# Kernel optimization log

Measured on AMD Instinct MI355X. Metric: run time of the kernel, lower is better.

## Reference

```python
import jax, jax.numpy as jnp
import numpy as np

N, D, M = 4096, 2048, 1000
NL = 2048
MAX_ITER = 5


def setup_inputs() -> dict:
    key = jax.random.key(0)
    k1, k2, k3 = jax.random.split(key, 3)
    fc7 = jax.random.normal(k1, (N, D), dtype=jnp.float32)
    # prior probs: softmax over random logits (row-stochastic, like CNN softmax output)
    probs = jax.nn.softmax(jax.random.normal(k2, (N, M), dtype=jnp.float32), axis=-1)
    labs = jax.random.randint(k3, (NL,), 0, M)
    L = jnp.arange(NL)
    U = jnp.arange(NL, N)
    return {"fc7": fc7, "probs": probs, "labs": labs, "L": L, "U": U}


def _get_W_correlation(fc7):
    # Pearson correlation between rows, negatives clipped to zero (set_negative='hard')
    x = fc7 - fc7.mean(axis=1, keepdims=True)
    norms = jnp.linalg.norm(x, axis=1)  # [n]
    W = (x @ x.T) / jnp.outer(norms, norms)  # [n, n]
    return jax.nn.relu(W)


def _init_probs_prior(probs, labs, L, U):
    n, m = probs.shape
    ps = jnp.zeros((n, m), dtype=probs.dtype)
    ps = ps.at[U].set(probs[U])       # unlabeled: CNN prior
    ps = ps.at[L, labs].set(1.0)      # labeled: one-hot
    return ps


def _replicator(W, ps, max_iter):
    def step(p, _):
        q = p * (W @ p)                              # [n, m]
        q = q / jnp.sum(q, axis=1, keepdims=True)
        return q, None
    ps, _ = jax.lax.scan(step, ps, None, length=max_iter)
    return ps


def reference(fc7, probs, labs, L, U):
    W = _get_W_correlation(fc7)
    ps = _init_probs_prior(probs, labs, L, U)
    ps = _replicator(W, ps, MAX_ITER)
    return ps, W
```

## Files before the change

### kernel.cpp

```cpp
#include <hip/hip_runtime.h>
#include <stdint.h>

#define NS 4096
#define DD 2048
#define MC 1000
#define MP 1024
#define NLAB 2048
#define NU 2048

typedef __attribute__((ext_vector_type(8))) short bf16x8;
typedef __attribute__((ext_vector_type(4))) float f32x4;

__device__ inline unsigned short f2bf(float f) {
  union { float f; uint32_t u; } v; v.f = f;
  uint32_t u = v.u;
  u = u + 0x7fffu + ((u >> 16) & 1u);
  return (unsigned short)(u >> 16);
}
__device__ inline float bf2f(unsigned short h) {
  union { uint32_t u; float f; } v; v.u = ((uint32_t)h) << 16;
  return v.f;
}

__device__ inline void gload_lds16(const void* g, void* l) {
  __builtin_amdgcn_global_load_lds(
      (const __attribute__((address_space(1))) void*)g,
      (__attribute__((address_space(3))) void*)l, 16, 0, 0);
}

__device__ inline float block_sum(float v, float* sm, int tid) {
  #pragma unroll
  for (int o = 32; o > 0; o >>= 1) v += __shfl_down(v, o, 64);
  __syncthreads();
  if ((tid & 63) == 0) sm[tid >> 6] = v;
  __syncthreads();
  return sm[0] + sm[1] + sm[2] + sm[3];
}

__global__ void center_norm_k(const float* __restrict__ fc7,
                              unsigned short* __restrict__ Xc,
                              float* __restrict__ invn) {
  __shared__ float sm[4];
  const int row = blockIdx.x;
  const int tid = threadIdx.x;
  const float4* src = (const float4*)(fc7 + (size_t)row * DD);
  float4 a = src[tid * 2];
  float4 b = src[tid * 2 + 1];
  float s = a.x + a.y + a.z + a.w + b.x + b.y + b.z + b.w;
  s = block_sum(s, sm, tid);
  const float mean = s * (1.f / (float)DD);
  float v0 = a.x - mean, v1 = a.y - mean, v2 = a.z - mean, v3 = a.w - mean;
  float v4 = b.x - mean, v5 = b.y - mean, v6 = b.z - mean, v7 = b.w - mean;
  float ss = v0*v0 + v1*v1 + v2*v2 + v3*v3 + v4*v4 + v5*v5 + v6*v6 + v7*v7;
  ss = block_sum(ss, sm, tid);
  if (tid == 0) invn[row] = rsqrtf(ss);
  ushort4 o0 = make_ushort4(f2bf(v0), f2bf(v1), f2bf(v2), f2bf(v3));
  ushort4 o1 = make_ushort4(f2bf(v4), f2bf(v5), f2bf(v6), f2bf(v7));
  ushort4* dst = (ushort4*)(Xc + (size_t)row * DD);
  dst[tid * 2] = o0;
  dst[tid * 2 + 1] = o1;
}

__global__ void gemm_w_sym(const unsigned short* __restrict__ A,
                           const float* __restrict__ invn,
                           float* __restrict__ outF,
                           unsigned short* __restrict__ outBF) {
  __shared__ __align__(16) unsigned short As[64 * 64];
  __shared__ __align__(16) unsigned short Bs[128 * 64];
  const int tid = threadIdx.x;
  const int wv = tid >> 6;
  const int ln = tid & 63;
  const int wr = wv >> 1, wc = wv & 1;

  int b = (blockIdx.x & 7) * 132 + (blockIdx.x >> 3);
  int r = 0;
  while (b >= 32 - (r >> 1)) { b -= 32 - (r >> 1); ++r; }
  const int c = (r >> 1) + b;
  const int rowBase = r * 64;
  const int colBase = c * 128;
  const bool mirror = (c > (r >> 1));
  const bool bfStraight = (colBase >= NLAB);
  const bool bfMirror = mirror && (rowBase >= NLAB);
  const int fr = ln & 15, kg = ln >> 4;

  f32x4 acc[2][4];
  f32x4 zz = {0.f, 0.f, 0.f, 0.f};
  #pragma unroll
  for (int i = 0; i < 2; ++i)
    #pragma unroll
    for (int j = 0; j < 4; ++j) acc[i][j] = zz;

  const int lrow = ln >> 3;
  const int lcol = ((ln & 7) ^ lrow) * 8;
  const unsigned short* Ap = A + (size_t)(rowBase + lrow) * DD + lcol;
  const unsigned short* Bp = A + (size_t)(colBase + lrow) * DD + lcol;

  for (int k0 = 0; k0 < DD; k0 += 64) {
    if (k0) __syncthreads();
    #pragma unroll
    for (int u = 0; u < 2; ++u) {
      const int rr = wv * 16 + u * 8;
      gload_lds16(Ap + (size_t)rr * DD + k0, &As[rr * 64]);
    }
    #pragma unroll
    for (int u = 0; u < 4; ++u) {
      const int rr = wv * 32 + u * 8;
      gload_lds16(Bp + (size_t)rr * DD + k0, &Bs[rr * 64]);
    }
    __syncthreads();
    #pragma unroll
    for (int kk = 0; kk < 2; ++kk) {
      bf16x8 af[2], bfr[4];
      #pragma unroll
      for (int i = 0; i < 2; ++i) {
        const int rr = wr * 32 + i * 16 + fr;
        af[i] = *(const bf16x8*)&As[rr * 64 + ((kk * 4 + kg) ^ (rr & 7)) * 8];
      }
      #pragma unroll
      for (int j = 0; j < 4; ++j) {
        const int rr = wc * 64 + j * 16 + fr;
        bfr[j] = *(const bf16x8*)&Bs[rr * 64 + ((kk * 4 + kg) ^ (rr & 7)) * 8];
      }
      #pragma unroll
      for (int i = 0; i < 2; ++i)
        #pragma unroll
        for (int j = 0; j < 4; ++j)
          acc[i][j] = __builtin_amdgcn_mfma_f32_16x16x32_bf16(af[i], bfr[j], acc[i][j], 0, 0, 0);
    }
  }

  const int cr = (ln >> 4) * 4;
  const int cc = ln & 15;
  #pragma unroll
  for (int i = 0; i < 2; ++i) {
    const int rb = rowBase + wr * 32 + i * 16 + cr;
    #pragma unroll
    for (int j = 0; j < 4; ++j) {
      const int cb = colBase + wc * 64 + j * 16 + cc;
      const float ic = invn[cb];
      float v[4];
      #pragma unroll
      for (int u = 0; u < 4; ++u) {
        float x = acc[i][j][u] * invn[rb + u] * ic;
        v[u] = x > 0.f ? x : 0.f;
        const size_t o = (size_t)(rb + u) * NS + cb;
        outF[o] = v[u];
        if (bfStraight) outBF[o] = f2bf(v[u]);
      }
      if (mirror) {
        const size_t o = (size_t)cb * NS + rb;
        *(float4*)&outF[o] = make_float4(v[0], v[1], v[2], v[3]);
        if (bfMirror)
          *(ushort4*)&outBF[o] = make_ushort4(f2bf(v[0]), f2bf(v[1]), f2bf(v[2]), f2bf(v[3]));
      }
    }
  }
}

__global__ void gemm_rep(const unsigned short* __restrict__ pT,
                         const unsigned short* __restrict__ Wbf,
                         float* __restrict__ q0, float* __restrict__ q1,
                         float* __restrict__ q2, float* __restrict__ q3,
                         int kBase) {
  __shared__ __align__(16) unsigned short As[64 * 64];
  __shared__ __align__(16) unsigned short Bs[128 * 64];
  const int tid = threadIdx.x;
  const int wv = tid >> 6;
  const int ln = tid & 63;
  const int wr = wv >> 1, wc = wv & 1;
  const int rowBase = blockIdx.y * 64;
  const int colBase = blockIdx.x * 128;
  const int kOff = kBase + blockIdx.z * 512;
  float* __restrict__ outF = (blockIdx.z == 0) ? q0 : (blockIdx.z == 1) ? q1
                           : (blockIdx.z == 2) ? q2 : q3;
  const int fr = ln & 15, kg = ln >> 4;

  f32x4 acc[2][4];
  f32x4 zz = {0.f, 0.f, 0.f, 0.f};
  #pragma unroll
  for (int i = 0; i < 2; ++i)
    #pragma unroll
    for (int j = 0; j < 4; ++j) acc[i][j] = zz;

  const int lrow = ln >> 3;
  const int lcol = ((ln & 7) ^ lrow) * 8;
  const unsigned short* Ap = pT + (size_t)(rowBase + lrow) * NS + kOff + lcol;
  const unsigned short* Bp = Wbf + (size_t)(NLAB + colBase + lrow) * NS + kOff + lcol;

  for (int k0 = 0; k0 < 512; k0 += 64) {
    if (k0) __syncthreads();
    #pragma unroll
    for (int u = 0; u < 2; ++u) {
      const int rr = wv * 16 + u * 8;
      gload_lds16(Ap + (size_t)rr * NS + k0, &As[rr * 64]);
    }
    #pragma unroll
    for (int u = 0; u < 4; ++u) {
      const int rr = wv * 32 + u * 8;
      gload_lds16(Bp + (size_t)rr * NS + k0, &Bs[rr * 64]);
    }
    __syncthreads();
    #pragma unroll
    for (int kk = 0; kk < 2; ++kk) {
      bf16x8 af[2], bfr[4];
      #pragma unroll
      for (int i = 0; i < 2; ++i) {
        const int rr = wr * 32 + i * 16 + fr;
        af[i] = *(const bf16x8*)&As[rr * 64 + ((kk * 4 + kg) ^ (rr & 7)) * 8];
      }
      #pragma unroll
      for (int j = 0; j < 4; ++j) {
        const int rr = wc * 64 + j * 16 + fr;
        bfr[j] = *(const bf16x8*)&Bs[rr * 64 + ((kk * 4 + kg) ^ (rr & 7)) * 8];
      }
      #pragma unroll
      for (int i = 0; i < 2; ++i)
        #pragma unroll
        for (int j = 0; j < 4; ++j)
          acc[i][j] = __builtin_amdgcn_mfma_f32_16x16x32_bf16(af[i], bfr[j], acc[i][j], 0, 0, 0);
    }
  }

  const int cr = (ln >> 4) * 4;
  const int cc = ln & 15;
  #pragma unroll
  for (int i = 0; i < 2; ++i) {
    const int rb = rowBase + wr * 32 + i * 16 + cr;
    #pragma unroll
    for (int j = 0; j < 4; ++j) {
      const int cb = colBase + wc * 64 + j * 16 + cc;
      #pragma unroll
      for (int u = 0; u < 4; ++u)
        outF[(size_t)(rb + u) * NU + cb] = acc[i][j][u];
    }
  }
}

__global__ void wl_gather_k(const int* __restrict__ labs,
                            const unsigned short* __restrict__ Wbf,
                            float* __restrict__ WL) {
  __shared__ unsigned long long masks[32];
  const int m = blockIdx.x;
  const int t = threadIdx.x;
  const int wv = t >> 6, ln = t & 63;
  #pragma unroll
  for (int u = 0; u < 8; ++u) {
    const int w2 = wv * 8 + u;
    unsigned long long msk = __ballot(labs[w2 * 64 + ln] == m);
    if (ln == 0) masks[w2] = msk;
  }
  __syncthreads();
  float acc[8] = {0.f, 0.f, 0.f, 0.f, 0.f, 0.f, 0.f, 0.f};
  for (int w2 = 0; w2 < 32; ++w2) {
    unsigned long long m64 = masks[w2];
    while (m64) {
      const int bit = __ffsll(m64) - 1;
      m64 &= (m64 - 1);
      const int j = w2 * 64 + bit;
      bf16x8 w = *(const bf16x8*)&Wbf[(size_t)j * NS + NLAB + t * 8];
      #pragma unroll
      for (int k = 0; k < 8; ++k) acc[k] += bf2f((unsigned short)w[k]);
    }
  }
  float* dst = WL + (size_t)m * NU + t * 8;
  *(float4*)dst = make_float4(acc[0], acc[1], acc[2], acc[3]);
  *(float4*)(dst + 4) = make_float4(acc[4], acc[5], acc[6], acc[7]);
}

__global__ void init_pT_k(const float* __restrict__ probs, const int* __restrict__ labs,
                          unsigned short* __restrict__ pT) {
  __shared__ float t[32][33];
  const int tx = threadIdx.x, ty = threadIdx.y;
  const int i0 = blockIdx.x * 32, m0 = blockIdx.y * 32;
  const int i = i0 + ty;
  const int m = m0 + tx;
  float v = 0.f;
  if (i < NLAB) v = (m == labs[i]) ? 1.f : 0.f;
  else if (m < MC) v = probs[(size_t)i * MC + m];
  t[ty][tx] = v;
  __syncthreads();
  pT[(size_t)(m0 + ty) * NS + i0 + tx] = f2bf(t[tx][ty]);
}

__global__ void onehot_k(const int* __restrict__ labs, float* __restrict__ ps) {
  const int i = blockIdx.x;
  const int m4 = threadIdx.x * 4;
  if (m4 >= MC) return;
  const int lab = labs[i];
  float4 v;
  v.x = (lab == m4)     ? 1.f : 0.f;
  v.y = (lab == m4 + 1) ? 1.f : 0.f;
  v.z = (lab == m4 + 2) ? 1.f : 0.f;
  v.w = (lab == m4 + 3) ? 1.f : 0.f;
  *(float4*)&ps[(size_t)i * MC + m4] = v;
}

__global__ void colsum_part_k(const float* __restrict__ q0, const float* __restrict__ q1,
                              const float* __restrict__ q2, const float* __restrict__ q3,
                              const float* __restrict__ WL,
                              const unsigned short* __restrict__ pT,
                              float* __restrict__ pq,
                              float* __restrict__ part) {
  const int i = blockIdx.x * 256 + threadIdx.x;
  const int c = blockIdx.y;
  float s = 0.f;
  #pragma unroll 4
  for (int mm = 0; mm < 64; ++mm) {
    const int m = c * 64 + mm;
    const size_t o = (size_t)m * NU + i;
    const float q = q0[o] + q1[o] + q2[o] + q3[o] + WL[o];
    const float f = bf2f(pT[(size_t)m * NS + NLAB + i]) * q;
    s += f;
    pq[o] = f;
  }
  part[c * NU + i] = s;
}

__global__ void colsum_fin_k(const float* __restrict__ part, float* __restrict__ rsum) {
  const int i = blockIdx.x * 256 + threadIdx.x;
  float s = 0.f;
  #pragma unroll
  for (int c = 0; c < 16; ++c) s += part[c * NU + i];
  rsum[i] = 1.0f / s;
}

__global__ void scale_k(const float* __restrict__ pq,
                        const float* __restrict__ rsum,
                        unsigned short* __restrict__ pT) {
  const int g = blockIdx.x * 256 + threadIdx.x;
  const int idx = g * 4;
  const int i = idx & (NU - 1);
  const int m = idx >> 11;
  float4 p = *(const float4*)(pq + idx);
  float4 r = *(const float4*)(rsum + i);
  ushort4 o = make_ushort4(f2bf(p.x * r.x), f2bf(p.y * r.y),
                           f2bf(p.z * r.z), f2bf(p.w * r.w));
  *(ushort4*)(pT + (size_t)m * NS + NLAB + i) = o;
}

__global__ void final_k(const float* __restrict__ pq,
                        const float* __restrict__ rsum,
                        float* __restrict__ ps) {
  __shared__ float t[32][33];
  const int tx = threadIdx.x, ty = threadIdx.y;
  const int i0 = blockIdx.x * 32, m0 = blockIdx.y * 32;
  t[ty][tx] = pq[(size_t)(m0 + ty) * NU + i0 + tx];
  __syncthreads();
  const int i = i0 + ty, m = m0 + tx;
  if (m < MC)
    ps[(size_t)(NLAB + i) * MC + m] = t[tx][ty] * rsum[i];
}

extern "C" void kernel_launch(void* const* d_in, const int* in_sizes, int n_in,
                              void* d_out, int out_size, void* d_ws, size_t ws_size,
                              hipStream_t stream) {
  const float* fc7   = (const float*)d_in[0];
  const float* probs = (const float*)d_in[1];
  const int*   labs  = (const int*)d_in[2];

  char* ws = (char*)d_ws;
  unsigned short* Xc   = (unsigned short*)(ws);
  unsigned short* Wbf  = (unsigned short*)(ws + (16ull << 20));
  unsigned short* pT   = (unsigned short*)(ws + (48ull << 20));
  float*          q0   = (float*)(ws + (56ull << 20));
  float*          q1   = (float*)(ws + (64ull << 20));
  float*          q2   = (float*)(ws + (72ull << 20));
  float*          q3   = (float*)(ws + (80ull << 20));
  float*          WL   = (float*)(ws + (88ull << 20));
  float*          pq   = (float*)(ws + (96ull << 20));
  float*          invn = (float*)(ws + (104ull << 20));
  float*          rsum = (float*)(ws + (104ull << 20) + (16ull << 10));
  float*          part = (float*)(ws + (105ull << 20));

  float* out_ps = (float*)d_out;
  float* out_W  = out_ps + (size_t)NS * MC;

  center_norm_k<<<NS, 256, 0, stream>>>(fc7, Xc, invn);

  gemm_w_sym<<<1056, 256, 0, stream>>>(Xc, invn, out_W, Wbf);

  init_pT_k<<<dim3(NS / 32, MP / 32), dim3(32, 32), 0, stream>>>(probs, labs, pT);
  onehot_k<<<NLAB, 256, 0, stream>>>(labs, out_ps);

  wl_gather_k<<<MP, 256, 0, stream>>>(labs, Wbf, WL);

  for (int it = 0; it < 5; ++it) {
    gemm_rep<<<dim3(NU / 128, MP / 64, 4), 256, 0, stream>>>(pT, Wbf, q0, q1, q2, q3, NLAB);
    colsum_part_k<<<dim3(NU / 256, 16), 256, 0, stream>>>(q0, q1, q2, q3, WL, pT, pq, part);
    colsum_fin_k<<<NU / 256, 256, 0, stream>>>(part, rsum);
    if (it < 4)
      scale_k<<<(MP * NU / 4) / 256, 256, 0, stream>>>(pq, rsum, pT);
    else
      final_k<<<dim3(NU / 32, MP / 32), dim3(32, 32), 0, stream>>>(pq, rsum, out_ps);
  }
}
```

Before: 266.2 us.

## Fuse row normalization into replicator GEMM A-tile load, drop scale kernel

Removes the per-iteration scale kernel that wrote a bf16 transposed probability buffer. The replicator GEMM now reads the unnormalized fp32 product buffer plus the reciprocal row sums, multiplies and converts to bf16 while staging the A tile into shared memory. The colsum kernel applies the pending scale itself, and ping-pong buffers carry the product and sums between iterations. This saves one launch and a full read/write pass per iteration, but the GEMM now does synchronous fp32 loads (twice the bytes) with conversion instead of direct-to-LDS bf16 loads, which can slow its inner loop.

```diff
diff --git a/kernel.cpp b/kernel.cpp
--- a/kernel.cpp
+++ b/kernel.cpp
@@ -157,11 +157,11 @@
   }
 }
 
-__global__ void gemm_rep(const unsigned short* __restrict__ pT,
+__global__ void gemm_rep(const float* __restrict__ pqP,
+                         const float* __restrict__ rsP,
                          const unsigned short* __restrict__ Wbf,
                          float* __restrict__ q0, float* __restrict__ q1,
-                         float* __restrict__ q2, float* __restrict__ q3,
-                         int kBase) {
+                         float* __restrict__ q2, float* __restrict__ q3) {
   __shared__ __align__(16) unsigned short As[64 * 64];
   __shared__ __align__(16) unsigned short Bs[128 * 64];
   const int tid = threadIdx.x;
@@ -170,7 +170,7 @@
   const int wr = wv >> 1, wc = wv & 1;
   const int rowBase = blockIdx.y * 64;
   const int colBase = blockIdx.x * 128;
-  const int kOff = kBase + blockIdx.z * 512;
+  const int kU = blockIdx.z * 512;
   float* __restrict__ outF = (blockIdx.z == 0) ? q0 : (blockIdx.z == 1) ? q1
                            : (blockIdx.z == 2) ? q2 : q3;
   const int fr = ln & 15, kg = ln >> 4;
@@ -182,17 +182,30 @@
     #pragma unroll
     for (int j = 0; j < 4; ++j) acc[i][j] = zz;
 
-  const int lrow = ln >> 3;
-  const int lcol = ((ln & 7) ^ lrow) * 8;
-  const unsigned short* Ap = pT + (size_t)(rowBase + lrow) * NS + kOff + lcol;
-  const unsigned short* Bp = Wbf + (size_t)(NLAB + colBase + lrow) * NS + kOff + lcol;
+  const int lr = ln >> 3;
+  const int sg = ln & 7;
+  const int sl = sg ^ lr;
+  const unsigned short* Bp = Wbf + (size_t)(NLAB + colBase + lr) * NS + NLAB + kU + sl * 8;
 
   for (int k0 = 0; k0 < 512; k0 += 64) {
     if (k0) __syncthreads();
-    #pragma unroll
-    for (int u = 0; u < 2; ++u) {
-      const int rr = wv * 16 + u * 8;
-      gload_lds16(Ap + (size_t)rr * NS + k0, &As[rr * 64]);
+    {
+      const float* rs = rsP + kU + k0 + sg * 8;
+      float4 r0 = *(const float4*)rs;
+      float4 r1 = *(const float4*)(rs + 4);
+      #pragma unroll
+      for (int u = 0; u < 2; ++u) {
+        const int rr = wv * 16 + u * 8 + lr;
+        const float* src = pqP + (size_t)(rowBase + rr) * NU + kU + k0 + sg * 8;
+        float4 a0 = *(const float4*)src;
+        float4 a1 = *(const float4*)(src + 4);
+        unsigned short hh[8];
+        hh[0] = f2bf(a0.x * r0.x); hh[1] = f2bf(a0.y * r0.y);
+        hh[2] = f2bf(a0.z * r0.z); hh[3] = f2bf(a0.w * r0.w);
+        hh[4] = f2bf(a1.x * r1.x); hh[5] = f2bf(a1.y * r1.y);
+        hh[6] = f2bf(a1.z * r1.z); hh[7] = f2bf(a1.w * r1.w);
+        *(bf16x8*)&As[rr * 64 + sl * 8] = *(bf16x8*)hh;
+      }
     }
     #pragma unroll
     for (int u = 0; u < 4; ++u) {
@@ -267,19 +280,19 @@
   *(float4*)(dst + 4) = make_float4(acc[4], acc[5], acc[6], acc[7]);
 }
 
-__global__ void init_pT_k(const float* __restrict__ probs, const int* __restrict__ labs,
-                          unsigned short* __restrict__ pT) {
+__global__ void init_pq_k(const float* __restrict__ probs, float* __restrict__ pq) {
   __shared__ float t[32][33];
   const int tx = threadIdx.x, ty = threadIdx.y;
   const int i0 = blockIdx.x * 32, m0 = blockIdx.y * 32;
   const int i = i0 + ty;
   const int m = m0 + tx;
-  float v = 0.f;
-  if (i < NLAB) v = (m == labs[i]) ? 1.f : 0.f;
-  else if (m < MC) v = probs[(size_t)i * MC + m];
-  t[ty][tx] = v;
+  t[ty][tx] = (m < MC) ? probs[(size_t)(NLAB + i) * MC + m] : 0.f;
   __syncthreads();
-  pT[(size_t)(m0 + ty) * NS + i0 + tx] = f2bf(t[tx][ty]);
+  pq[(size_t)(m0 + ty) * NU + i0 + tx] = t[tx][ty];
+}
+
+__global__ void init_rs_k(float* __restrict__ rs) {
+  rs[blockIdx.x * 256 + threadIdx.x] = 1.0f;
 }
 
 __global__ void onehot_k(const int* __restrict__ labs, float* __restrict__ ps) {
@@ -298,20 +311,22 @@
 __global__ void colsum_part_k(const float* __restrict__ q0, const float* __restrict__ q1,
                               const float* __restrict__ q2, const float* __restrict__ q3,
                               const float* __restrict__ WL,
-                              const unsigned short* __restrict__ pT,
-                              float* __restrict__ pq,
+                              const float* __restrict__ pqP,
+                              const float* __restrict__ rsP,
+                              float* __restrict__ pqC,
                               float* __restrict__ part) {
   const int i = blockIdx.x * 256 + threadIdx.x;
   const int c = blockIdx.y;
+  const float rsv = rsP[i];
   float s = 0.f;
   #pragma unroll 4
   for (int mm = 0; mm < 64; ++mm) {
     const int m = c * 64 + mm;
     const size_t o = (size_t)m * NU + i;
     const float q = q0[o] + q1[o] + q2[o] + q3[o] + WL[o];
-    const float f = bf2f(pT[(size_t)m * NS + NLAB + i]) * q;
+    const float f = (pqP[o] * rsv) * q;
     s += f;
-    pq[o] = f;
+    pqC[o] = f;
   }
   part[c * NU + i] = s;
 }
@@ -322,20 +337,6 @@
   #pragma unroll
   for (int c = 0; c < 16; ++c) s += part[c * NU + i];
   rsum[i] = 1.0f / s;
-}
-
-__global__ void scale_k(const float* __restrict__ pq,
-                        const float* __restrict__ rsum,
-                        unsigned short* __restrict__ pT) {
-  const int g = blockIdx.x * 256 + threadIdx.x;
-  const int idx = g * 4;
-  const int i = idx & (NU - 1);
-  const int m = idx >> 11;
-  float4 p = *(const float4*)(pq + idx);
-  float4 r = *(const float4*)(rsum + i);
-  ushort4 o = make_ushort4(f2bf(p.x * r.x), f2bf(p.y * r.y),
-                           f2bf(p.z * r.z), f2bf(p.w * r.w));
-  *(ushort4*)(pT + (size_t)m * NS + NLAB + i) = o;
 }
 
 __global__ void final_k(const float* __restrict__ pq,
@@ -361,36 +362,43 @@
   char* ws = (char*)d_ws;
   unsigned short* Xc   = (unsigned short*)(ws);
   unsigned short* Wbf  = (unsigned short*)(ws + (16ull << 20));
-  unsigned short* pT   = (unsigned short*)(ws + (48ull << 20));
-  float*          q0   = (float*)(ws + (56ull << 20));
-  float*          q1   = (float*)(ws + (64ull << 20));
-  float*          q2   = (float*)(ws + (72ull << 20));
-  float*          q3   = (float*)(ws + (80ull << 20));
-  float*          WL   = (float*)(ws + (88ull << 20));
-  float*          pq   = (float*)(ws + (96ull << 20));
+  float*          q0   = (float*)(ws + (48ull << 20));
+  float*          q1   = (float*)(ws + (56ull << 20));
+  float*          q2   = (float*)(ws + (64ull << 20));
+  float*          q3   = (float*)(ws + (72ull << 20));
+  float*          WL   = (float*)(ws + (80ull << 20));
+  float*          pqA  = (float*)(ws + (88ull << 20));
+  float*          pqB  = (float*)(ws + (96ull << 20));
   float*          invn = (float*)(ws + (104ull << 20));
-  float*          rsum = (float*)(ws + (104ull << 20) + (16ull << 10));
+  float*          rsA  = (float*)(ws + (104ull << 20) + (16ull << 10));
+  float*          rsB  = (float*)(ws + (104ull << 20) + (32ull << 10));
   float*          part = (float*)(ws + (105ull << 20));
 
   float* out_ps = (float*)d_out;
   float* out_W  = out_ps + (size_t)NS * MC;
 
+  float* pqbuf[2] = {pqA, pqB};
+  float* rsbuf[2] = {rsA, rsB};
+
   center_norm_k<<<NS, 256, 0, stream>>>(fc7, Xc, invn);
 
   gemm_w_sym<<<1056, 256, 0, stream>>>(Xc, invn, out_W, Wbf);
 
-  init_pT_k<<<dim3(NS / 32, MP / 32), dim3(32, 32), 0, stream>>>(probs, labs, pT);
+  init_pq_k<<<dim3(NU / 32, MP / 32), dim3(32, 32), 0, stream>>>(probs, pqA);
+  init_rs_k<<<NU / 256, 256, 0, stream>>>(rsA);
   onehot_k<<<NLAB, 256, 0, stream>>>(labs, out_ps);
 
   wl_gather_k<<<MP, 256, 0, stream>>>(labs, Wbf, WL);
 
   for (int it = 0; it < 5; ++it) {
-    gemm_rep<<<dim3(NU / 128, MP / 64, 4), 256, 0, stream>>>(pT, Wbf, q0, q1, q2, q3, NLAB);
-    colsum_part_k<<<dim3(NU / 256, 16), 256, 0, stream>>>(q0, q1, q2, q3, WL, pT, pq, part);
-    colsum_fin_k<<<NU / 256, 256, 0, stream>>>(part, rsum);
-    if (it < 4)
-      scale_k<<<(MP * NU / 4) / 256, 256, 0, stream>>>(pq, rsum, pT);
-    else
-      final_k<<<dim3(NU / 32, MP / 32), dim3(32, 32), 0, stream>>>(pq, rsum, out_ps);
-  }
-}
+    float* pqP = pqbuf[it & 1];
+    float* rsP = rsbuf[it & 1];
+    float* pqC = pqbuf[(it + 1) & 1];
+    float* rsC = rsbuf[(it + 1) & 1];
+    gemm_rep<<<dim3(NU / 128, MP / 64, 4), 256, 0, stream>>>(pqP, rsP, Wbf, q0, q1, q2, q3);
+    colsum_part_k<<<dim3(NU / 256, 16), 256, 0, stream>>>(q0, q1, q2, q3, WL, pqP, rsP, pqC, part);
+    colsum_fin_k<<<NU / 256, 256, 0, stream>>>(part, rsC);
+    if (it == 4)
+      final_k<<<dim3(NU / 32, MP / 32), dim3(32, 32), 0, stream>>>(pqC, rsC, out_ps);
+  }
+}
```

New measurement: 295.1 us. +10.8%, slower.
